# Performance work log

Hardware: AMD Instinct MI355X
Metric: run time of the kernel (lower is better)

## Reference

```python
import jax, jax.numpy as jnp
import numpy as np

T, N, E, H, G, P = 8, 512, 64, 128, 4, 128
NS = 2.0  # neighbourhood_size


def _init(k, shape):
    fan_in = shape[-1]
    return jax.random.normal(k, shape, jnp.float32) / jnp.sqrt(jnp.float32(fan_in))


def setup_inputs() -> dict:
    key = jax.random.key(0)
    ks = jax.random.split(key, 12)
    return {
        "observed": jax.random.normal(ks[0], (T, N, 2), jnp.float32),
        "W_pos": _init(ks[1], (E, 2)), "b_pos": jnp.zeros((E,), jnp.float32),
        "W_pool": _init(ks[2], (P, G * G * H)), "b_pool": jnp.zeros((P,), jnp.float32),
        "W_ih_enc": _init(ks[3], (4 * H, E + P)), "b_ih_enc": jnp.zeros((4 * H,), jnp.float32),
        "W_hh_enc": _init(ks[4], (4 * H, H)), "b_hh_enc": jnp.zeros((4 * H,), jnp.float32),
        "W_ih_dec": _init(ks[5], (4 * H, E + P)), "b_ih_dec": jnp.zeros((4 * H,), jnp.float32),
        "W_hh_dec": _init(ks[6], (4 * H, H)), "b_hh_dec": jnp.zeros((4 * H,), jnp.float32),
        "W_out": _init(ks[7], (2, H)), "b_out": jnp.zeros((2,), jnp.float32),
        "n_predict": 12,
    }


def _impute(observed):
    # backfill leading gaps, forward-fill later gaps, zeros if never valid
    Tn, n, _ = observed.shape
    finite = jnp.isfinite(observed).all(-1)                       # [T,N]
    idx = jnp.where(finite, jnp.arange(Tn)[:, None], -1)
    last = jax.lax.associative_scan(jnp.maximum, idx, axis=0)     # last valid t' <= t
    first = jnp.argmax(finite, axis=0)                            # first valid t
    take = jnp.where(last >= 0, last, first[None, :])             # [T,N]
    obs = jnp.take_along_axis(observed, jnp.broadcast_to(take[:, :, None], (Tn, n, 2)), axis=0)
    return jnp.where(finite.any(0)[None, :, None], obs, 0.0)


def _social_pool(pos, hidden, W_pool, b_pool):
    # grid-cell binning + per-cell max pooling of neighbour hidden states
    n, h = hidden.shape
    half, cell = NS / 2.0, NS / G
    rel = pos[None, :, :] - pos[:, None, :]                       # [N,N,2] pos[j]-pos[i]
    fin_pos = jnp.isfinite(pos).all(-1)
    fin_hid = jnp.isfinite(hidden).all(-1)
    inr = (jnp.abs(rel) <= half).all(-1)
    eye = jnp.eye(n, dtype=bool)
    mask = inr & fin_pos[:, None] & fin_pos[None, :] & fin_hid[None, :] & (~eye)
    g = jnp.clip(jnp.floor((rel + half) / cell).astype(jnp.int32), 0, G - 1)  # [N,N,2]
    cid = g[..., 0] * G + g[..., 1]                               # gx*G+gy layout
    seg = jnp.where(mask, jnp.arange(n, dtype=jnp.int32)[:, None] * (G * G) + cid, n * G * G)
    seg = seg.reshape(-1)                                         # [N*N]
    data = jnp.broadcast_to(hidden[None], (n, n, h)).reshape(n * n, h)
    pooled = jax.ops.segment_max(data, seg, num_segments=n * G * G + 1)[: n * G * G]
    counts = jax.ops.segment_sum(jnp.ones((n * n,), jnp.float32), seg, num_segments=n * G * G + 1)[: n * G * G]
    pooled = jnp.where(counts[:, None] > 0, pooled, 0.0)          # empty cells -> zero_hidden
    grid = pooled.reshape(n, G * G * h)
    return jax.nn.relu(grid @ W_pool.T + b_pool)


def reference(observed, W_pos, b_pos, W_pool, b_pool,
              W_ih_enc, b_ih_enc, W_hh_enc, b_hh_enc,
              W_ih_dec, b_ih_dec, W_hh_dec, b_hh_dec,
              W_out, b_out, n_predict):
    obs = _impute(observed)
    n = obs.shape[1]

    def step(W_ih, b_ih, W_hh, b_hh, hs, cs, pos, prev):
        vel = pos - prev
        emb = jax.nn.relu(vel @ W_pos.T + b_pos)
        soc = _social_pool(pos, hs, W_pool, b_pool)
        x = jnp.concatenate([emb, soc], axis=1)
        gates = x @ W_ih.T + b_ih + hs @ W_hh.T + b_hh
        i, f, gg, o = jnp.split(gates, 4, axis=1)
        cs2 = jax.nn.sigmoid(f) * cs + jax.nn.sigmoid(i) * jnp.tanh(gg)
        hs2 = jax.nn.sigmoid(o) * jnp.tanh(cs2)
        nxt = pos + hs2 @ W_out.T + b_out
        return hs2, cs2, nxt

    def enc_step(carry, inp):
        hs, cs = carry
        pos, prev = inp
        hs, cs, _ = step(W_ih_enc, b_ih_enc, W_hh_enc, b_hh_enc, hs, cs, pos, prev)
        return (hs, cs), None

    hs = jnp.zeros((n, H), jnp.float32)
    cs = jnp.zeros((n, H), jnp.float32)
    (hs, cs), _ = jax.lax.scan(enc_step, (hs, cs), (obs[1:], obs[:-1]))

    def dec_step(carry, _):
        hs, cs, prev, curr = carry
        hs, cs, nxt = step(W_ih_dec, b_ih_dec, W_hh_dec, b_hh_dec, hs, cs, curr, prev)
        return (hs, cs, jax.lax.stop_gradient(curr), jax.lax.stop_gradient(nxt)), nxt

    _, preds = jax.lax.scan(dec_step, (hs, cs, obs[-1], obs[-1]), None, length=int(n_predict))
    return preds  # [n_predict, N, 2]
```

## Files before the change

### kernel.cpp

```cpp
#include <hip/hip_runtime.h>
#include <math.h>

#define NBLK 256
#define NTHR 512

#define OFF_OBS     8256
#define OFF_HS      16448
#define OFF_PART    81984
#define OFF_WTPOOL  606272
#define OFF_WTG_E   868416
#define OFF_WTG_D   1032256

#define LDS_BYTES 30848

typedef float vf4 __attribute__((ext_vector_type(4)));
typedef float vf2 __attribute__((ext_vector_type(2)));

__device__ __forceinline__ void st_bypass_f4(float* p, vf4 v) {
    asm volatile("global_store_dwordx4 %0, %1, off sc0 sc1" :: "v"(p), "v"(v) : "memory");
}
__device__ __forceinline__ void st_bypass_f2(float* p, vf2 v) {
    asm volatile("global_store_dwordx2 %0, %1, off sc0 sc1" :: "v"(p), "v"(v) : "memory");
}
__device__ __forceinline__ vf4 ld_bypass_f4(const float* p) {
    vf4 v;
    asm volatile("global_load_dwordx4 %0, %1, off sc0 sc1\n\ts_waitcnt vmcnt(0)"
                 : "=&v"(v) : "v"(p) : "memory");
    return v;
}
__device__ __forceinline__ void ld_bypass_f4x8(const float* b, int stride, vf4* v) {
    asm volatile(
        "global_load_dwordx4 %0, %8, off sc0 sc1\n\t"
        "global_load_dwordx4 %1, %9, off sc0 sc1\n\t"
        "global_load_dwordx4 %2, %10, off sc0 sc1\n\t"
        "global_load_dwordx4 %3, %11, off sc0 sc1\n\t"
        "global_load_dwordx4 %4, %12, off sc0 sc1\n\t"
        "global_load_dwordx4 %5, %13, off sc0 sc1\n\t"
        "global_load_dwordx4 %6, %14, off sc0 sc1\n\t"
        "global_load_dwordx4 %7, %15, off sc0 sc1\n\t"
        "s_waitcnt vmcnt(0)"
        : "=&v"(v[0]), "=&v"(v[1]), "=&v"(v[2]), "=&v"(v[3]),
          "=&v"(v[4]), "=&v"(v[5]), "=&v"(v[6]), "=&v"(v[7])
        : "v"(b), "v"(b + stride), "v"(b + 2 * stride), "v"(b + 3 * stride),
          "v"(b + 4 * stride), "v"(b + 5 * stride), "v"(b + 6 * stride), "v"(b + 7 * stride)
        : "memory");
}
__device__ __forceinline__ vf2 ld_llc_f2(const float* p) {
    union { unsigned long long u; vf2 f; } cv;
    cv.u = __hip_atomic_load((const unsigned long long*)p, __ATOMIC_RELAXED,
                             __HIP_MEMORY_SCOPE_AGENT);
    return cv.f;
}
__device__ __forceinline__ float ld_cohere(const float* p) {
    return __hip_atomic_load(p, __ATOMIC_RELAXED, __HIP_MEMORY_SCOPE_AGENT);
}

__device__ __forceinline__ void grid_barrier_fenced(unsigned* flags, unsigned* gen, unsigned seq) {
    __syncthreads();
    if (threadIdx.x == 0)
        __builtin_amdgcn_fence(__ATOMIC_RELEASE, "agent");
    if (blockIdx.x == 0) {
        if (threadIdx.x < 64) {
            #pragma unroll
            for (int q = 0; q < 4; q++) {
                int bb = threadIdx.x * 4 + q;
                if (bb != 0) {
                    while (__hip_atomic_load(&flags[bb * 16], __ATOMIC_RELAXED,
                                             __HIP_MEMORY_SCOPE_AGENT) != seq)
                        __builtin_amdgcn_s_sleep(1);
                }
            }
        }
        __syncthreads();
        if (threadIdx.x == 0) {
            __hip_atomic_store(gen, seq, __ATOMIC_RELAXED, __HIP_MEMORY_SCOPE_AGENT);
            __builtin_amdgcn_fence(__ATOMIC_ACQUIRE, "agent");
        }
    } else {
        if (threadIdx.x == 0) {
            __hip_atomic_store(&flags[blockIdx.x * 16], seq, __ATOMIC_RELAXED,
                               __HIP_MEMORY_SCOPE_AGENT);
            while (__hip_atomic_load(gen, __ATOMIC_RELAXED,
                                     __HIP_MEMORY_SCOPE_AGENT) != seq)
                __builtin_amdgcn_s_sleep(2);
            __builtin_amdgcn_fence(__ATOMIC_ACQUIRE, "agent");
        }
    }
    __syncthreads();
}

__device__ __forceinline__ void grid_barrier_nf(unsigned* flags, unsigned* gen, unsigned seq) {
    __syncthreads();
    if (blockIdx.x == 0) {
        if (threadIdx.x < 64) {
            #pragma unroll
            for (int q = 0; q < 4; q++) {
                int bb = threadIdx.x * 4 + q;
                if (bb != 0) {
                    while (__hip_atomic_load(&flags[bb * 16], __ATOMIC_RELAXED,
                                             __HIP_MEMORY_SCOPE_AGENT) != seq)
                        __builtin_amdgcn_s_sleep(1);
                }
            }
        }
        __syncthreads();
        if (threadIdx.x == 0)
            __hip_atomic_store(gen, seq, __ATOMIC_RELAXED, __HIP_MEMORY_SCOPE_AGENT);
    } else {
        if (threadIdx.x == 0) {
            __hip_atomic_store(&flags[blockIdx.x * 16], seq, __ATOMIC_RELAXED,
                               __HIP_MEMORY_SCOPE_AGENT);
            while (__hip_atomic_load(gen, __ATOMIC_RELAXED,
                                     __HIP_MEMORY_SCOPE_AGENT) != seq)
                __builtin_amdgcn_s_sleep(2);
        }
    }
    __syncthreads();
}

__device__ __forceinline__ float sigm(float x) { return 1.f / (1.f + expf(-x)); }

__global__ void __launch_bounds__(NTHR, 1) social_lstm(
    const float* __restrict__ observed,
    const float* __restrict__ W_pos, const float* __restrict__ b_pos,
    const float* __restrict__ W_pool, const float* __restrict__ b_pool,
    const float* __restrict__ Wih_e, const float* __restrict__ bih_e,
    const float* __restrict__ Whh_e, const float* __restrict__ bhh_e,
    const float* __restrict__ Wih_d, const float* __restrict__ bih_d,
    const float* __restrict__ Whh_d, const float* __restrict__ bhh_d,
    const float* __restrict__ W_out, const float* __restrict__ b_out,
    float* __restrict__ out, float* __restrict__ ws, int npred)
{
    extern __shared__ char smem_raw[];
    const int t = threadIdx.x, b = blockIdx.x;
    const int gid = b * NTHR + t;

    unsigned* flags  = (unsigned*)ws;
    unsigned* gen    = flags + 4096;
    unsigned* cnt_rt = flags + 4352;
    float* obs     = ws + OFF_OBS;
    float* hs      = ws + OFF_HS;
    float* part    = ws + OFF_PART;
    float* Wt_pool = ws + OFF_WTPOOL;
    float* Wt_ge   = ws + OFF_WTG_E;
    float* Wt_gd   = ws + OFF_WTG_D;
    unsigned seq = 1;

    if (gid < 65536) hs[gid] = 0.f;
    if (gid < 512) {
        float vx[8], vy[8];
        int fin = 0;
        for (int tt = 0; tt < 8; tt++) {
            float x = observed[tt * 1024 + gid * 2];
            float y = observed[tt * 1024 + gid * 2 + 1];
            vx[tt] = x; vy[tt] = y;
            if (isfinite(x) && isfinite(y)) fin |= (1 << tt);
        }
        int firstv = -1;
        for (int tt = 7; tt >= 0; tt--) if (fin & (1 << tt)) firstv = tt;
        int last = -1;
        for (int tt = 0; tt < 8; tt++) {
            if (fin & (1 << tt)) last = tt;
            int take = (last >= 0) ? last : firstv;
            float ox = 0.f, oy = 0.f;
            if (take >= 0) { ox = vx[take]; oy = vy[take]; }
            obs[tt * 1024 + gid * 2]     = ox;
            obs[tt * 1024 + gid * 2 + 1] = oy;
        }
    }
    if (gid < 65536) {
        int p = gid >> 9, k4 = gid & 511;
        float4 v = *(const float4*)(W_pool + p * 2048 + k4 * 4);
        float* dst = Wt_pool + (k4 * 4) * 128 + p;
        dst[0] = v.x; dst[128] = v.y; dst[256] = v.z; dst[384] = v.w;
    }
    for (int idx = gid; idx < 163840; idx += NBLK * NTHR) {
        int k = idx >> 9, o = idx & 511;
        float ve, vd;
        if (k < 192) { ve = Wih_e[o * 192 + k];       vd = Wih_d[o * 192 + k]; }
        else         { ve = Whh_e[o * 128 + k - 192]; vd = Whh_d[o * 128 + k - 192]; }
        Wt_ge[idx] = ve; Wt_gd[idx] = vd;
    }
    grid_barrier_fenced(flags, gen, seq++);

    const int rt = b >> 3, kc = b & 7, hc = kc;
    const int R0 = rt * 16;
    float cs_reg = 0.f;
    const int nstep = 7 + npred;

    for (int s = 0; s < nstep; s++) {
        const float* posp  = (s < 7) ? (obs + (s + 1) * 1024)
                                     : ((s == 7) ? (obs + 7 * 1024) : (out + (s - 8) * 1024));
        const float* prevp = (s < 7) ? (obs + s * 1024)
                                     : ((s <= 8) ? (obs + 7 * 1024) : (out + (s - 9) * 1024));
        const float* Wt_g = (s < 7) ? Wt_ge : Wt_gd;
        const float* bihp = (s < 7) ? bih_e : bih_d;
        const float* bhhp = (s < 7) ? bhh_e : bhh_d;

        {
            float* pos2 = (float*)smem_raw;
            int* cnt    = (int*)(smem_raw + 4096);
            unsigned short* lst = (unsigned short*)(smem_raw + 4224);
            float* AsT  = (float*)(smem_raw + 10368);

            if (t < 256) {
                if (s < 8) ((float4*)pos2)[t] = ((const float4*)posp)[t];
                else       ((vf4*)pos2)[t] = ld_bypass_f4(posp + t * 4);
            }
            if (t < 32) cnt[t] = 0;
            __syncthreads();

            if (kc == 1 && s >= 7 && t < 16) {
                int i = R0 + t;
                vf2 v;
                v.x = pos2[2 * i] + b_out[0];
                v.y = pos2[2 * i + 1] + b_out[1];
                st_bypass_f2(out + (s - 7) * 1024 + 2 * i, v);
            }
            {
                int a = t >> 5, i = R0 + a;
                float pix = pos2[2 * i], piy = pos2[2 * i + 1];
                int c0 = kc * 2;
                for (int jj = 0; jj < 16; jj++) {
                    int j = (t & 31) + jj * 32;
                    float dx = pos2[2 * j]     - pix;
                    float dy = pos2[2 * j + 1] - piy;
                    if (j != i && fabsf(dx) <= 1.0f && fabsf(dy) <= 1.0f) {
                        int gx = (int)floorf((dx + 1.0f) * 2.0f); gx = gx < 0 ? 0 : (gx > 3 ? 3 : gx);
                        int gy = (int)floorf((dy + 1.0f) * 2.0f); gy = gy < 0 ? 0 : (gy > 3 ? 3 : gy);
                        int cc = gx * 4 + gy - c0;
                        if (cc == 0 || cc == 1) {
                            int slot = atomicAdd(&cnt[a * 2 + cc], 1);
                            if (slot < 96) lst[(a * 2 + cc) * 96 + slot] = (unsigned short)j;
                        }
                    }
                }
            }
            __syncthreads();
            {
                int a = t >> 5, cc = (t >> 4) & 1, hq = t & 15;
                int len = cnt[a * 2 + cc]; if (len > 96) len = 96;
                float m[8];
                #pragma unroll
                for (int u = 0; u < 8; u++) m[u] = -3.0e38f;
                for (int e = 0; e < len; e++) {
                    int j = lst[(a * 2 + cc) * 96 + e];
                    const float* hr = hs + j * 128 + hq * 8;
                    vf2 p0 = ld_llc_f2(hr);
                    vf2 p1 = ld_llc_f2(hr + 2);
                    vf2 p2 = ld_llc_f2(hr + 4);
                    vf2 p3 = ld_llc_f2(hr + 6);
                    m[0] = fmaxf(m[0], p0.x); m[1] = fmaxf(m[1], p0.y);
                    m[2] = fmaxf(m[2], p1.x); m[3] = fmaxf(m[3], p1.y);
                    m[4] = fmaxf(m[4], p2.x); m[5] = fmaxf(m[5], p2.y);
                    m[6] = fmaxf(m[6], p3.x); m[7] = fmaxf(m[7], p3.y);
                }
                #pragma unroll
                for (int u = 0; u < 8; u++)
                    AsT[(cc * 128 + hq * 8 + u) * 20 + a] = (len > 0) ? m[u] : 0.f;
            }
            __syncthreads();
            {
                int og = (t & 7) | (((t >> 6) & 1) << 3);
                int ks = (t >> 3) & 7;
                int rowg = t >> 7;
                float acc[4][8];
                #pragma unroll
                for (int r = 0; r < 4; r++)
                    #pragma unroll
                    for (int o = 0; o < 8; o++) acc[r][o] = 0.f;
                const float4* W4 = (const float4*)Wt_pool;
                int kb = kc * 256 + ks * 32;
                #pragma unroll 4
                for (int kk = 0; kk < 32; kk++) {
                    int kl = ks * 32 + kk;
                    float4 a4 = *(const float4*)&AsT[kl * 20 + rowg * 4];
                    float4 w0 = W4[(kb + kk) * 32 + og * 2];
                    float4 w1 = W4[(kb + kk) * 32 + og * 2 + 1];
                    float ar[4] = {a4.x, a4.y, a4.z, a4.w};
                    float wo[8] = {w0.x, w0.y, w0.z, w0.w, w1.x, w1.y, w1.z, w1.w};
                    #pragma unroll
                    for (int r = 0; r < 4; r++)
                        #pragma unroll
                        for (int o = 0; o < 8; o++)
                            acc[r][o] = fmaf(ar[r], wo[o], acc[r][o]);
                }
                #pragma unroll
                for (int r = 0; r < 4; r++)
                    #pragma unroll
                    for (int o = 0; o < 8; o++) {
                        acc[r][o] += __shfl_xor(acc[r][o], 8);
                        acc[r][o] += __shfl_xor(acc[r][o], 16);
                        acc[r][o] += __shfl_xor(acc[r][o], 32);
                    }
                if ((t & 56) == 0) {
                    #pragma unroll
                    for (int r = 0; r < 4; r++) {
                        int row = R0 + rowg * 4 + r;
                        float* pp = part + kc * 65536 + row * 128 + og * 8;
                        vf4 lo, hi;
                        lo.x = acc[r][0]; lo.y = acc[r][1]; lo.z = acc[r][2]; lo.w = acc[r][3];
                        hi.x = acc[r][4]; hi.y = acc[r][5]; hi.z = acc[r][6]; hi.w = acc[r][7];
                        st_bypass_f4(pp,     lo);
                        st_bypass_f4(pp + 4, hi);
                    }
                }
            }
        }

        __syncthreads();
        if (t == 0) {
            __hip_atomic_fetch_add(&cnt_rt[rt * 16], 1u, __ATOMIC_RELAXED, __HIP_MEMORY_SCOPE_AGENT);
            unsigned tgt = 8u * (unsigned)(s + 1);
            while (__hip_atomic_load(&cnt_rt[rt * 16], __ATOMIC_RELAXED,
                                     __HIP_MEMORY_SCOPE_AGENT) != tgt)
                __builtin_amdgcn_s_sleep(1);
        }
        __syncthreads();

        {
            float* AsT  = (float*)smem_raw;
            float* red  = (float*)(smem_raw + 25600);
            float* hrow = (float*)(smem_raw + 29696);
            {
                int r = t >> 5, e2 = (t & 31) * 2;
                int i2 = 2 * (R0 + r);
                float vx = ld_cohere(posp + i2)     - ld_cohere(prevp + i2);
                float vy = ld_cohere(posp + i2 + 1) - ld_cohere(prevp + i2 + 1);
                float e0 = fmaxf(W_pos[e2 * 2]     * vx + W_pos[e2 * 2 + 1] * vy + b_pos[e2],     0.f);
                float e1 = fmaxf(W_pos[e2 * 2 + 2] * vx + W_pos[e2 * 2 + 3] * vy + b_pos[e2 + 1], 0.f);
                AsT[(e2 + 0) * 20 + r] = e0;
                AsT[(e2 + 1) * 20 + r] = e1;
            }
            {
                int r = t >> 5, p4 = (t & 31) * 4;
                vf4 pv[8];
                ld_bypass_f4x8(part + (R0 + r) * 128 + p4, 65536, pv);
                float sv[4] = {0.f, 0.f, 0.f, 0.f};
                #pragma unroll
                for (int kc2 = 0; kc2 < 8; kc2++) {
                    sv[0] += pv[kc2].x; sv[1] += pv[kc2].y;
                    sv[2] += pv[kc2].z; sv[3] += pv[kc2].w;
                }
                #pragma unroll
                for (int u = 0; u < 4; u++)
                    AsT[(64 + p4 + u) * 20 + r] = fmaxf(sv[u] + b_pool[p4 + u], 0.f);
            }
            {
                int r = t >> 5, h4 = (t & 31) * 4;
                vf4 v = ld_bypass_f4(hs + (R0 + r) * 128 + h4);
                AsT[(192 + h4 + 0) * 20 + r] = v.x;
                AsT[(192 + h4 + 1) * 20 + r] = v.y;
                AsT[(192 + h4 + 2) * 20 + r] = v.z;
                AsT[(192 + h4 + 3) * 20 + r] = v.w;
            }
            __syncthreads();
            {
                int og = (t & 7) | (((t >> 6) & 1) << 3);
                int ks = (t >> 3) & 7;
                int rowg = t >> 7;
                int col4 = (og >> 2) * 32 + hc * 4 + (og & 3);
                float acc[4][4];
                #pragma unroll
                for (int r = 0; r < 4; r++)
                    #pragma unroll
                    for (int o = 0; o < 4; o++) acc[r][o] = 0.f;
                const float4* Wg4 = (const float4*)Wt_g;
                #pragma unroll 4
                for (int kk = 0; kk < 40; kk++) {
                    int k = ks * 40 + kk;
                    float4 a4 = *(const float4*)&AsT[k * 20 + rowg * 4];
                    float4 w  = Wg4[k * 128 + col4];
                    float ar[4] = {a4.x, a4.y, a4.z, a4.w};
                    float wo[4] = {w.x, w.y, w.z, w.w};
                    #pragma unroll
                    for (int r = 0; r < 4; r++)
                        #pragma unroll
                        for (int o = 0; o < 4; o++)
                            acc[r][o] = fmaf(ar[r], wo[o], acc[r][o]);
                }
                #pragma unroll
                for (int r = 0; r < 4; r++)
                    #pragma unroll
                    for (int o = 0; o < 4; o++) {
                        acc[r][o] += __shfl_xor(acc[r][o], 8);
                        acc[r][o] += __shfl_xor(acc[r][o], 16);
                        acc[r][o] += __shfl_xor(acc[r][o], 32);
                    }
                if ((t & 56) == 0) {
                    #pragma unroll
                    for (int r = 0; r < 4; r++)
                        *(float4*)&red[(rowg * 4 + r) * 64 + og * 4] =
                            make_float4(acc[r][0], acc[r][1], acc[r][2], acc[r][3]);
                }
            }
            __syncthreads();
            if (t < 256) {
                int rl = t >> 4, hh = t & 15;
                float g4[4];
                #pragma unroll
                for (int q = 0; q < 4; q++) {
                    int colq = q * 128 + hc * 16 + hh;
                    g4[q] = red[rl * 64 + q * 16 + hh] + bihp[colq] + bhhp[colq];
                }
                float si = sigm(g4[0]);
                float sf = sigm(g4[1]);
                float so = sigm(g4[3]);
                float c2 = sf * cs_reg + si * tanhf(g4[2]);
                float h2 = so * tanhf(c2);
                cs_reg = c2;
                hrow[rl * 16 + hh] = h2;
                if (s >= 7) {
                    int i = R0 + rl, h = hc * 16 + hh;
                    float v0 = W_out[h] * h2;
                    float v1 = W_out[128 + h] * h2;
                    v0 += __shfl_down(v0, 8); v0 += __shfl_down(v0, 4);
                    v0 += __shfl_down(v0, 2); v0 += __shfl_down(v0, 1);
                    v1 += __shfl_down(v1, 8); v1 += __shfl_down(v1, 4);
                    v1 += __shfl_down(v1, 2); v1 += __shfl_down(v1, 1);
                    if (hh == 0) {
                        atomicAdd(&out[(s - 7) * 1024 + 2 * i],     v0);
                        atomicAdd(&out[(s - 7) * 1024 + 2 * i + 1], v1);
                    }
                }
            }
            __syncthreads();
            if (t < 64) {
                int rl = t >> 2, q = t & 3;
                vf4 v;
                v.x = hrow[rl * 16 + q * 4 + 0];
                v.y = hrow[rl * 16 + q * 4 + 1];
                v.z = hrow[rl * 16 + q * 4 + 2];
                v.w = hrow[rl * 16 + q * 4 + 3];
                st_bypass_f4(hs + (R0 + rl) * 128 + hc * 16 + q * 4, v);
            }
        }
        grid_barrier_nf(flags, gen, seq++);
    }
}

extern "C" void kernel_launch(void* const* d_in, const int* in_sizes, int n_in,
                              void* d_out, int out_size, void* d_ws, size_t ws_size,
                              hipStream_t stream) {
    const float* observed = (const float*)d_in[0];
    const float* W_pos    = (const float*)d_in[1];
    const float* b_pos    = (const float*)d_in[2];
    const float* W_pool   = (const float*)d_in[3];
    const float* b_pool   = (const float*)d_in[4];
    const float* Wih_e    = (const float*)d_in[5];
    const float* bih_e    = (const float*)d_in[6];
    const float* Whh_e    = (const float*)d_in[7];
    const float* bhh_e    = (const float*)d_in[8];
    const float* Wih_d    = (const float*)d_in[9];
    const float* bih_d    = (const float*)d_in[10];
    const float* Whh_d    = (const float*)d_in[11];
    const float* bhh_d    = (const float*)d_in[12];
    const float* W_out    = (const float*)d_in[13];
    const float* b_out    = (const float*)d_in[14];
    float* outp = (float*)d_out;
    float* wsp  = (float*)d_ws;
    int npred = out_size / 1024;

    hipMemsetAsync(d_ws, 0, 33024, stream);

    social_lstm<<<NBLK, NTHR, LDS_BYTES, stream>>>(
        observed, W_pos, b_pos, W_pool, b_pool,
        Wih_e, bih_e, Whh_e, bhh_e,
        Wih_d, bih_d, Whh_d, bhh_d,
        W_out, b_out, outp, wsp, npred);
}
```

Before: 690.6 us.

## Batch neighbour gathers into wide loads and replace counter barrier with per-chunk flags

The pooling max loop now gathers eight neighbour hidden-state rows per iteration with 16 wide cache-bypassing loads issued together, instead of four dependent 8-byte atomic loads per neighbour, which gives more memory-level parallelism. The per-row-tile atomic counter barrier becomes per-chunk flag stores. Blocks now compute the embedding and hidden-state staging before spinning on those flags, so the wait overlaps useful work. Padding the last batch with duplicate indices adds some redundant loads, and the flag protocol depends on a release fence that is not shown.

```diff
diff --git a/kernel.cpp b/kernel.cpp
--- a/kernel.cpp
+++ b/kernel.cpp
@@ -45,11 +45,33 @@
           "v"(b + 4 * stride), "v"(b + 5 * stride), "v"(b + 6 * stride), "v"(b + 7 * stride)
         : "memory");
 }
-__device__ __forceinline__ vf2 ld_llc_f2(const float* p) {
-    union { unsigned long long u; vf2 f; } cv;
-    cv.u = __hip_atomic_load((const unsigned long long*)p, __ATOMIC_RELAXED,
-                             __HIP_MEMORY_SCOPE_AGENT);
-    return cv.f;
+__device__ __forceinline__ void ld_gather8(
+    const float* a0, const float* a1, const float* a2, const float* a3,
+    const float* a4, const float* a5, const float* a6, const float* a7, vf4* v) {
+    asm volatile(
+        "global_load_dwordx4 %0, %16, off sc0 sc1\n\t"
+        "global_load_dwordx4 %1, %16, off offset:16 sc0 sc1\n\t"
+        "global_load_dwordx4 %2, %17, off sc0 sc1\n\t"
+        "global_load_dwordx4 %3, %17, off offset:16 sc0 sc1\n\t"
+        "global_load_dwordx4 %4, %18, off sc0 sc1\n\t"
+        "global_load_dwordx4 %5, %18, off offset:16 sc0 sc1\n\t"
+        "global_load_dwordx4 %6, %19, off sc0 sc1\n\t"
+        "global_load_dwordx4 %7, %19, off offset:16 sc0 sc1\n\t"
+        "global_load_dwordx4 %8, %20, off sc0 sc1\n\t"
+        "global_load_dwordx4 %9, %20, off offset:16 sc0 sc1\n\t"
+        "global_load_dwordx4 %10, %21, off sc0 sc1\n\t"
+        "global_load_dwordx4 %11, %21, off offset:16 sc0 sc1\n\t"
+        "global_load_dwordx4 %12, %22, off sc0 sc1\n\t"
+        "global_load_dwordx4 %13, %22, off offset:16 sc0 sc1\n\t"
+        "global_load_dwordx4 %14, %23, off sc0 sc1\n\t"
+        "global_load_dwordx4 %15, %23, off offset:16 sc0 sc1\n\t"
+        "s_waitcnt vmcnt(0)"
+        : "=&v"(v[0]), "=&v"(v[1]), "=&v"(v[2]), "=&v"(v[3]),
+          "=&v"(v[4]), "=&v"(v[5]), "=&v"(v[6]), "=&v"(v[7]),
+          "=&v"(v[8]), "=&v"(v[9]), "=&v"(v[10]), "=&v"(v[11]),
+          "=&v"(v[12]), "=&v"(v[13]), "=&v"(v[14]), "=&v"(v[15])
+        : "v"(a0), "v"(a1), "v"(a2), "v"(a3), "v"(a4), "v"(a5), "v"(a6), "v"(a7)
+        : "memory");
 }
 __device__ __forceinline__ float ld_cohere(const float* p) {
     return __hip_atomic_load(p, __ATOMIC_RELAXED, __HIP_MEMORY_SCOPE_AGENT);
@@ -137,7 +159,7 @@
 
     unsigned* flags  = (unsigned*)ws;
     unsigned* gen    = flags + 4096;
-    unsigned* cnt_rt = flags + 4352;
+    unsigned* rtf    = flags + 4112;
     float* obs     = ws + OFF_OBS;
     float* hs      = ws + OFF_HS;
     float* part    = ws + OFF_PART;
@@ -243,17 +265,24 @@
                 float m[8];
                 #pragma unroll
                 for (int u = 0; u < 8; u++) m[u] = -3.0e38f;
-                for (int e = 0; e < len; e++) {
-                    int j = lst[(a * 2 + cc) * 96 + e];
-                    const float* hr = hs + j * 128 + hq * 8;
-                    vf2 p0 = ld_llc_f2(hr);
-                    vf2 p1 = ld_llc_f2(hr + 2);
-                    vf2 p2 = ld_llc_f2(hr + 4);
-                    vf2 p3 = ld_llc_f2(hr + 6);
-                    m[0] = fmaxf(m[0], p0.x); m[1] = fmaxf(m[1], p0.y);
-                    m[2] = fmaxf(m[2], p1.x); m[3] = fmaxf(m[3], p1.y);
-                    m[4] = fmaxf(m[4], p2.x); m[5] = fmaxf(m[5], p2.y);
-                    m[6] = fmaxf(m[6], p3.x); m[7] = fmaxf(m[7], p3.y);
+                const unsigned short* ll = lst + (a * 2 + cc) * 96;
+                for (int e = 0; e < len; e += 8) {
+                    const float* ap[8];
+                    #pragma unroll
+                    for (int k2 = 0; k2 < 8; k2++) {
+                        int ee = e + k2; if (ee >= len) ee = len - 1;
+                        ap[k2] = hs + (int)ll[ee] * 128 + hq * 8;
+                    }
+                    vf4 v[16];
+                    ld_gather8(ap[0], ap[1], ap[2], ap[3], ap[4], ap[5], ap[6], ap[7], v);
+                    #pragma unroll
+                    for (int k2 = 0; k2 < 8; k2++) {
+                        vf4 lo = v[2 * k2], hi = v[2 * k2 + 1];
+                        m[0] = fmaxf(m[0], lo.x); m[1] = fmaxf(m[1], lo.y);
+                        m[2] = fmaxf(m[2], lo.z); m[3] = fmaxf(m[3], lo.w);
+                        m[4] = fmaxf(m[4], hi.x); m[5] = fmaxf(m[5], hi.y);
+                        m[6] = fmaxf(m[6], hi.z); m[7] = fmaxf(m[7], hi.w);
+                    }
                 }
                 #pragma unroll
                 for (int u = 0; u < 8; u++)
@@ -309,19 +338,11 @@
         }
 
         __syncthreads();
-        if (t == 0) {
-            __hip_atomic_fetch_add(&cnt_rt[rt * 16], 1u, __ATOMIC_RELAXED, __HIP_MEMORY_SCOPE_AGENT);
-            unsigned tgt = 8u * (unsigned)(s + 1);
-            while (__hip_atomic_load(&cnt_rt[rt * 16], __ATOMIC_RELAXED,
-                                     __HIP_MEMORY_SCOPE_AGENT) != tgt)
-                __builtin_amdgcn_s_sleep(1);
-        }
-        __syncthreads();
-
+        if (t == 0)
+            __hip_atomic_store(&rtf[(rt * 8 + kc) * 16], (unsigned)(s + 1),
+                               __ATOMIC_RELAXED, __HIP_MEMORY_SCOPE_AGENT);
         {
             float* AsT  = (float*)smem_raw;
-            float* red  = (float*)(smem_raw + 25600);
-            float* hrow = (float*)(smem_raw + 29696);
             {
                 int r = t >> 5, e2 = (t & 31) * 2;
                 int i2 = 2 * (R0 + r);
@@ -333,20 +354,6 @@
                 AsT[(e2 + 1) * 20 + r] = e1;
             }
             {
-                int r = t >> 5, p4 = (t & 31) * 4;
-                vf4 pv[8];
-                ld_bypass_f4x8(part + (R0 + r) * 128 + p4, 65536, pv);
-                float sv[4] = {0.f, 0.f, 0.f, 0.f};
-                #pragma unroll
-                for (int kc2 = 0; kc2 < 8; kc2++) {
-                    sv[0] += pv[kc2].x; sv[1] += pv[kc2].y;
-                    sv[2] += pv[kc2].z; sv[3] += pv[kc2].w;
-                }
-                #pragma unroll
-                for (int u = 0; u < 4; u++)
-                    AsT[(64 + p4 + u) * 20 + r] = fmaxf(sv[u] + b_pool[p4 + u], 0.f);
-            }
-            {
                 int r = t >> 5, h4 = (t & 31) * 4;
                 vf4 v = ld_bypass_f4(hs + (R0 + r) * 128 + h4);
                 AsT[(192 + h4 + 0) * 20 + r] = v.x;
@@ -354,7 +361,29 @@
                 AsT[(192 + h4 + 2) * 20 + r] = v.z;
                 AsT[(192 + h4 + 3) * 20 + r] = v.w;
             }
-            __syncthreads();
+            if (t < 8) {
+                while (__hip_atomic_load(&rtf[(rt * 8 + t) * 16], __ATOMIC_RELAXED,
+                                         __HIP_MEMORY_SCOPE_AGENT) != (unsigned)(s + 1))
+                    __builtin_amdgcn_s_sleep(1);
+            }
+            __syncthreads();
+            {
+                int r = t >> 5, p4 = (t & 31) * 4;
+                vf4 pv[8];
+                ld_bypass_f4x8(part + (R0 + r) * 128 + p4, 65536, pv);
+                float sv[4] = {0.f, 0.f, 0.f, 0.f};
+                #pragma unroll
+                for (int kc2 = 0; kc2 < 8; kc2++) {
+                    sv[0] += pv[kc2].x; sv[1] += pv[kc2].y;
+                    sv[2] += pv[kc2].z; sv[3] += pv[kc2].w;
+                }
+                #pragma unroll
+                for (int u = 0; u < 4; u++)
+                    AsT[(64 + p4 + u) * 20 + r] = fmaxf(sv[u] + b_pool[p4 + u], 0.f);
+            }
+            __syncthreads();
+            float* red  = (float*)(smem_raw + 25600);
+            float* hrow = (float*)(smem_raw + 29696);
             {
                 int og = (t & 7) | (((t >> 6) & 1) << 3);
                 int ks = (t >> 3) & 7;
```

Result: faster. 651.8 us (-5.6%).
